# Performance work log

Measured on AMD Instinct MI355X. Metric: run time of the kernel, lower is better.

The kernel has to match this reference:

```python
import jax, jax.numpy as jnp
import numpy as np

T_STEPS = 100
T_EMB = 16
EPS = 1e-8


def sin_emb(t, dim):
    # sinusoidal_time_embedding: [cos(t*f), sin(t*f)] with f = exp(-log(1e4)*i/half)
    half = dim // 2
    freqs = jnp.exp(-jnp.log(jnp.float32(10000.0)) * jnp.arange(half, dtype=jnp.float32) / half)
    a = t.astype(jnp.float32)[:, None] * freqs[None, :]
    return jnp.concatenate([jnp.cos(a), jnp.sin(a)], axis=-1)


def lstm_layer(x_tbf, W_ih, W_hh, b):
    # x_tbf: [T, B, F]; torch gate order i, f, g, o
    B = x_tbf.shape[1]
    H = W_hh.shape[1]

    def step(carry, x_t):
        h, c = carry
        g = x_t @ W_ih.T + h @ W_hh.T + b
        i, f, gg, o = jnp.split(g, 4, axis=-1)
        c = jax.nn.sigmoid(f) * c + jax.nn.sigmoid(i) * jnp.tanh(gg)
        h = jax.nn.sigmoid(o) * jnp.tanh(c)
        return (h, c), h

    z = jnp.zeros((B, H), x_tbf.dtype)
    (h, c), ys = jax.lax.scan(step, (z, z), x_tbf)
    return ys, h


def _forward(x_hist, x_future, y0, turb_idx, pred_steps, init_noise, turb_emb,
             W_ih0, W_hh0, b_ih0, b_hh0, W_ih1, W_hh1, b_ih1, b_hh1,
             W1, b1, W2, b2, W3, b3):
    betas = jnp.linspace(1e-4, 0.02, T_STEPS).astype(jnp.float32)
    alphas = 1.0 - betas
    alpha_bars = jnp.cumprod(alphas)

    B = x_hist.shape[0]
    emb = turb_emb[turb_idx]  # [B, E]
    eh = jnp.broadcast_to(emb[:, None, :], (B, x_hist.shape[1], emb.shape[1]))
    ef = jnp.broadcast_to(emb[:, None, :], (B, x_future.shape[1], emb.shape[1]))
    xh = jnp.concatenate([x_hist, eh], axis=-1).transpose(1, 0, 2)    # [T_in, B, F+E]
    xf = jnp.concatenate([x_future, ef], axis=-1).transpose(1, 0, 2)  # [P, B, exo+E]

    ys0, _ = lstm_layer(xh, W_ih0, W_hh0, b_ih0 + b_hh0)
    _, enc_out = lstm_layer(ys0, W_ih1, W_hh1, b_ih1 + b_hh1)         # [B, H] = h[-1]

    def mlp(x):
        h = jax.nn.relu(x @ W1.T + b1)
        h = jax.nn.relu(h @ W2.T + b2)
        return h @ W3.T + b3

    def ar_step(prev_y, xs):
        exo_t, step, y_init = xs
        cond = jnp.concatenate([enc_out, exo_t, prev_y], axis=1)  # [B, cond_dim]
        h_e = sin_emb(jnp.full((B,), step), T_EMB)

        def dstep(y, t):
            t_e = sin_emb(jnp.full((B,), t), T_EMB)
            eps_hat = mlp(jnp.concatenate([cond, y, t_e, h_e], axis=1))  # [B,1]
            b_t, a_t, ab_t = betas[t], alphas[t], alpha_bars[t]
            pred_x0 = (y - jnp.sqrt(1.0 - ab_t) * eps_hat) / (jnp.sqrt(ab_t) + EPS)
            mean = (y - b_t / (jnp.sqrt(1.0 - ab_t) + EPS) * eps_hat) / (jnp.sqrt(a_t) + EPS)
            # eval mode -> deterministic sampling: posterior noise term is zero
            return jnp.where(t == 0, pred_x0, mean), None

        y, _ = jax.lax.scan(dstep, y_init, jnp.arange(T_STEPS - 1, -1, -1))
        return y, y[:, 0]

    _, seq = jax.lax.scan(ar_step, y0, (xf, jnp.arange(pred_steps), init_noise))
    return seq.T[:, :, None]  # [B, pred_steps, 1]


def setup_inputs() -> dict:
    key = jax.random.key(0)
    ks = list(jax.random.split(key, 24))
    kit = iter(ks)
    B, T_IN, F_IN, EXO, EMB, PRED, HID, NTURB = 1024, 96, 8, 6, 16, 8, 128, 100
    in0 = F_IN + EMB                 # 24
    cond_dim = HID + EXO + EMB + 1   # 151
    in_mlp = cond_dim + 1 + T_EMB + T_EMB  # 184

    def nrm(shape, s=0.05):
        return jax.random.normal(next(kit), shape, jnp.float32) * s

    return {
        'x_hist': jax.random.normal(next(kit), (B, T_IN, F_IN), jnp.float32),
        'x_future': jax.random.normal(next(kit), (B, PRED, EXO), jnp.float32),
        'y0': jnp.zeros((B, 1), jnp.float32),
        'turb_idx': jax.random.randint(next(kit), (B,), 0, NTURB),
        'pred_steps': PRED,
        'init_noise': jax.random.normal(next(kit), (PRED, B, 1), jnp.float32),
        'turb_emb': nrm((NTURB, EMB), 0.1),
        'W_ih0': nrm((4 * HID, in0)), 'W_hh0': nrm((4 * HID, HID)),
        'b_ih0': jnp.zeros((4 * HID,), jnp.float32), 'b_hh0': jnp.zeros((4 * HID,), jnp.float32),
        'W_ih1': nrm((4 * HID, HID)), 'W_hh1': nrm((4 * HID, HID)),
        'b_ih1': jnp.zeros((4 * HID,), jnp.float32), 'b_hh1': jnp.zeros((4 * HID,), jnp.float32),
        'W1': nrm((HID, in_mlp)), 'b1': jnp.zeros((HID,), jnp.float32),
        'W2': nrm((HID, HID)), 'b2': jnp.zeros((HID,), jnp.float32),
        'W3': nrm((1, HID)), 'b3': jnp.zeros((1,), jnp.float32),
    }


def reference(x_hist, x_future, y0, turb_idx, pred_steps, init_noise, turb_emb,
              W_ih0, W_hh0, b_ih0, b_hh0, W_ih1, W_hh1, b_ih1, b_hh1,
              W1, b1, W2, b2, W3, b3):
    return _forward(x_hist, x_future, y0, turb_idx, pred_steps, init_noise, turb_emb,
                    W_ih0, W_hh0, b_ih0, b_hh0, W_ih1, W_hh1, b_ih1, b_hh1,
                    W1, b1, W2, b2, W3, b3)
```

## Files before the change

kernel.cpp:

```cpp
#include <hip/hip_runtime.h>
#include <hip/hip_fp16.h>
#include <stdint.h>


typedef __attribute__((ext_vector_type(2))) _Float16 half2_t;
typedef __attribute__((ext_vector_type(8))) _Float16 v8h;
typedef __attribute__((ext_vector_type(4))) float v4f;

#define DEV __device__ __forceinline__

DEV uint32_t pack2f(float a, float b) {
  __half ha = __float2half_rn(a), hb = __float2half_rn(b);
  return (uint32_t)__half_as_ushort(ha) | ((uint32_t)__half_as_ushort(hb) << 16);
}

DEV float2 up2(uint32_t u) {
  half2_t h = __builtin_bit_cast(half2_t, u);
  return make_float2((float)h.x, (float)h.y);
}

DEV float fast_ex2(float x) {
#if __has_builtin(__builtin_amdgcn_exp2f)
  return __builtin_amdgcn_exp2f(x);
#else
  return exp2f(x);
#endif
}
DEV float fast_rcp(float x) {
#if __has_builtin(__builtin_amdgcn_rcpf)
  return __builtin_amdgcn_rcpf(x);
#else
  return 1.f / x;
#endif
}
DEV float sigm(float x) { return fast_rcp(1.f + fast_ex2(-1.4426950408889634f * x)); }
DEV float tanh_f(float x) {
  return 2.f * fast_rcp(1.f + fast_ex2(-2.8853900817779268f * x)) - 1.f;
}

DEV uint32_t pk_add(uint32_t a, uint32_t b) {
  return __builtin_bit_cast(uint32_t,
      __builtin_bit_cast(half2_t, a) + __builtin_bit_cast(half2_t, b));
}

DEV uint32_t pk_relufma(uint32_t w, uint32_t y, uint32_t b) {
  half2_t r = __builtin_bit_cast(half2_t, w) * __builtin_bit_cast(half2_t, y) +
              __builtin_bit_cast(half2_t, b);
  half2_t z = {(_Float16)0.f, (_Float16)0.f};
#if __has_builtin(__builtin_elementwise_max)
  r = __builtin_elementwise_max(r, z);
#else
  uint32_t u = __builtin_bit_cast(uint32_t, r);
  uint32_t mask = ((u >> 15) & 1u) * 0xFFFFu | ((u >> 31) & 1u) * 0xFFFF0000u;
  r = __builtin_bit_cast(half2_t, u & ~mask);
#endif
  return __builtin_bit_cast(uint32_t, r);
}

DEV uint32_t pk_max0(uint32_t a) {
  half2_t z = {(_Float16)0.f, (_Float16)0.f};
#if __has_builtin(__builtin_elementwise_max)
  return __builtin_bit_cast(uint32_t,
      __builtin_elementwise_max(__builtin_bit_cast(half2_t, a), z));
#else
  uint32_t mask = ((a >> 15) & 1u) * 0xFFFFu | ((a >> 31) & 1u) * 0xFFFF0000u;
  return a & ~mask;
#endif
}

DEV uint32_t cvtpk(float y) {
#if __has_builtin(__builtin_amdgcn_cvt_pkrtz)
  return __builtin_bit_cast(uint32_t, __builtin_amdgcn_cvt_pkrtz(y, y));
#else
  return pack2f(y, y);
#endif
}

DEV uint32_t cvtpk2(float a, float b) {
#if __has_builtin(__builtin_amdgcn_cvt_pkrtz)
  return __builtin_bit_cast(uint32_t, __builtin_amdgcn_cvt_pkrtz(a, b));
#else
  return pack2f(a, b);
#endif
}

DEV half2_t pk_fma2(uint32_t a, uint32_t b, half2_t c) {
  return __builtin_bit_cast(half2_t, a) * __builtin_bit_cast(half2_t, b) + c;
}

static constexpr size_t OFF_XH  = 0;
static constexpr size_t OFF_W0  = 4718592;
static constexpr size_t OFF_BS0 = 4882432;
static constexpr size_t OFF_W1L = 4884480;
static constexpr size_t OFF_BS1 = 5146624;
static constexpr size_t OFF_W2P = 5148672;
static constexpr size_t OFF_ENC = 5181440;
static constexpr size_t OFF_YS0 = 5705728;

__global__ void k_prep_xh(const float* __restrict__ xh, const int* __restrict__ tix,
                          const float* __restrict__ temb, uint32_t* __restrict__ out) {
  int idx = blockIdx.x * 256 + threadIdx.x;
  if (idx >= 96 * 1024 * 12) return;
  int m = idx % 12;
  int tb = idx / 12;
  int b = tb & 1023, t = tb >> 10;
  int k0 = 2 * m, k1 = k0 + 1;
  float v0 = (k0 < 8) ? xh[(b * 96 + t) * 8 + k0] : temb[tix[b] * 16 + (k0 - 8)];
  float v1 = (k1 < 8) ? xh[(b * 96 + t) * 8 + k1] : temb[tix[b] * 16 + (k1 - 8)];
  out[idx] = pack2f(v0, v1);
}

__global__ void k_prep_w(const float* __restrict__ Wih0, const float* __restrict__ Whh0,
                         const float* __restrict__ bih0, const float* __restrict__ bhh0,
                         const float* __restrict__ Wih1, const float* __restrict__ Whh1,
                         const float* __restrict__ bih1, const float* __restrict__ bhh1,
                         const float* __restrict__ W2,
                         uint32_t* __restrict__ w0p, uint32_t* __restrict__ w1p,
                         uint32_t* __restrict__ w2p, float* __restrict__ bs0,
                         float* __restrict__ bs1) {
  int idx = blockIdx.x * 256 + threadIdx.x;
  if (idx < 40960) {
    int w = idx / 5120;
    int r = idx % 5120;
    int T = r / 1280; r %= 1280;
    int f = r / 256;  r %= 256;
    int l = r >> 2, c = r & 3;
    int m = l & 15, qf = l >> 4;
    int g = (m & 3) * 128 + w * 16 + (m >> 2) * 4 + T;
    int k0 = f * 32 + qf * 8 + 2 * c, k1 = k0 + 1;
    float a = (k0 < 24) ? Wih0[g * 24 + k0] : ((k0 < 152) ? Whh0[g * 128 + k0 - 24] : 0.f);
    float b = (k1 < 24) ? Wih0[g * 24 + k1] : ((k1 < 152) ? Whh0[g * 128 + k1 - 24] : 0.f);
    w0p[idx] = pack2f(a, b);
  } else if (idx < 106496) {
    int i = idx - 40960;
    int w = i / 8192;
    int r = i % 8192;
    int T = r / 2048; r %= 2048;
    int f = r / 256;  r %= 256;
    int l = r >> 2, c = r & 3;
    int m = l & 15, qf = l >> 4;
    int g = (m & 3) * 128 + w * 16 + (m >> 2) * 4 + T;
    int k0 = f * 32 + qf * 8 + 2 * c, k1 = k0 + 1;
    float a = (k0 < 128) ? Wih1[g * 128 + k0] : Whh1[g * 128 + k0 - 128];
    float b = (k1 < 128) ? Wih1[g * 128 + k1] : Whh1[g * 128 + k1 - 128];
    w1p[i] = pack2f(a, b);
  } else if (idx < 114688) {
    int i = idx - 106496;
    w2p[i] = pack2f(W2[2 * i], W2[2 * i + 1]);
  } else if (idx < 115200) {
    int i = idx - 114688;
    bs0[i] = bih0[i] + bhh0[i];
  } else if (idx < 115712) {
    int i = idx - 115200;
    bs1[i] = bih1[i] + bhh1[i];
  }
}

__global__ __launch_bounds__(512, 2) void k_lstm0(const uint32_t* __restrict__ xh16,
                                                  const uint32_t* __restrict__ w0A,
                                                  const float* __restrict__ bs0,
                                                  __half* __restrict__ ys0) {
  __shared__ __align__(16) __half inb[2][16][160];
  const int tid = threadIdx.x;
  const int w = tid >> 6, l = tid & 63;
  const int n = l & 15, ql = l >> 4;
  const int ju = w * 16 + ql * 4;
  const int bbase = blockIdx.x * 16;

  uint4 Af[4][5];
#pragma unroll
  for (int T = 0; T < 4; T++)
#pragma unroll
    for (int f = 0; f < 5; f++)
      Af[T][f] = ((const uint4*)w0A)[((w * 4 + T) * 5 + f) * 64 + l];
  float bias[4][4];
#pragma unroll
  for (int T = 0; T < 4; T++)
#pragma unroll
    for (int r = 0; r < 4; r++) bias[T][r] = bs0[r * 128 + ju + T];

  for (int i = tid; i < 2560; i += 512) ((uint32_t*)inb)[i] = 0u;
  __syncthreads();
  if (tid < 192) {
    int b = tid / 12, m = tid % 12;
    ((uint32_t*)&inb[0][b][0])[m] = xh16[(0 * 1024 + bbase + b) * 12 + m];
  }
  float cst[4] = {0.f, 0.f, 0.f, 0.f};
  __syncthreads();

  for (int t = 0; t < 96; t++) {
    const int cur = t & 1, nxt = cur ^ 1;
    uint32_t sx = 0;
    int sb = 0, sm = 0;
    if (t < 95 && tid < 192) {
      sb = tid / 12; sm = tid % 12;
      sx = xh16[((t + 1) * 1024 + bbase + sb) * 12 + sm];
    }
    v4f acc[4];
#pragma unroll
    for (int T = 0; T < 4; T++) acc[T] = (v4f){0.f, 0.f, 0.f, 0.f};
#pragma unroll
    for (int f = 0; f < 5; f++) {
      uint4 bu = *(const uint4*)&inb[cur][n][f * 32 + ql * 8];
      v8h Bv = __builtin_bit_cast(v8h, bu);
#pragma unroll
      for (int T = 0; T < 4; T++)
        acc[T] = __builtin_amdgcn_mfma_f32_16x16x32_f16(
            __builtin_bit_cast(v8h, Af[T][f]), Bv, acc[T], 0, 0, 0);
    }
    float hv[4];
#pragma unroll
    for (int T = 0; T < 4; T++) {
      float gi = acc[T][0] + bias[T][0];
      float gf = acc[T][1] + bias[T][1];
      float gg = acc[T][2] + bias[T][2];
      float go = acc[T][3] + bias[T][3];
      float c = sigm(gf) * cst[T] + sigm(gi) * tanh_f(gg);
      cst[T] = c;
      hv[T] = sigm(go) * tanh_f(c);
    }
    uint32_t h01 = pack2f(hv[0], hv[1]), h23 = pack2f(hv[2], hv[3]);
    *(uint2*)&inb[nxt][n][24 + ju] = make_uint2(h01, h23);
    *(uint2*)((__half*)ys0 + (size_t)(t * 1024 + bbase + n) * 128 + ju) = make_uint2(h01, h23);
    if (t < 95 && tid < 192) ((uint32_t*)&inb[nxt][sb][0])[sm] = sx;
    __syncthreads();
  }
}

__global__ __launch_bounds__(512, 2) void k_lstm1(const uint32_t* __restrict__ ys0u,
                                                  const uint32_t* __restrict__ w1A,
                                                  const float* __restrict__ bs1,
                                                  float* __restrict__ enc) {
  __shared__ __align__(16) __half inb[2][16][264];
  const int tid = threadIdx.x;
  const int w = tid >> 6, l = tid & 63;
  const int n = l & 15, ql = l >> 4;
  const int ju = w * 16 + ql * 4;
  const int bbase = blockIdx.x * 16;
  const int sb = tid >> 5, sc = tid & 31;

  uint4 Af[4][8];
#pragma unroll
  for (int T = 0; T < 4; T++)
#pragma unroll
    for (int f = 0; f < 8; f++)
      Af[T][f] = ((const uint4*)w1A)[((w * 4 + T) * 8 + f) * 64 + l];
  float bias[4][4];
#pragma unroll
  for (int T = 0; T < 4; T++)
#pragma unroll
    for (int r = 0; r < 4; r++) bias[T][r] = bs1[r * 128 + ju + T];

  for (int i = tid; i < 4224; i += 512) ((uint32_t*)inb)[i] = 0u;
  __syncthreads();
  {
    uint2 v = ((const uint2*)ys0u)[(size_t)(0 * 1024 + bbase + sb) * 32 + sc];
    *(uint2*)&inb[0][sb][sc * 4] = v;
  }
  float cst[4] = {0.f, 0.f, 0.f, 0.f};
  __syncthreads();

  for (int t = 0; t < 96; t++) {
    const int cur = t & 1, nxt = cur ^ 1;
    uint2 sv = make_uint2(0u, 0u);
    if (t < 95)
      sv = ((const uint2*)ys0u)[(size_t)((t + 1) * 1024 + bbase + sb) * 32 + sc];
    v4f acc[4];
#pragma unroll
    for (int T = 0; T < 4; T++) acc[T] = (v4f){0.f, 0.f, 0.f, 0.f};
#pragma unroll
    for (int f = 0; f < 8; f++) {
      uint4 bu = *(const uint4*)&inb[cur][n][f * 32 + ql * 8];
      v8h Bv = __builtin_bit_cast(v8h, bu);
#pragma unroll
      for (int T = 0; T < 4; T++)
        acc[T] = __builtin_amdgcn_mfma_f32_16x16x32_f16(
            __builtin_bit_cast(v8h, Af[T][f]), Bv, acc[T], 0, 0, 0);
    }
    float hv[4];
#pragma unroll
    for (int T = 0; T < 4; T++) {
      float gi = acc[T][0] + bias[T][0];
      float gf = acc[T][1] + bias[T][1];
      float gg = acc[T][2] + bias[T][2];
      float go = acc[T][3] + bias[T][3];
      float c = sigm(gf) * cst[T] + sigm(gi) * tanh_f(gg);
      cst[T] = c;
      hv[T] = sigm(go) * tanh_f(c);
    }
    *(uint2*)&inb[nxt][n][128 + ju] = make_uint2(pack2f(hv[0], hv[1]), pack2f(hv[2], hv[3]));
    if (t < 95) *(uint2*)&inb[nxt][sb][sc * 4] = sv;
    if (t == 95)
      *(float4*)&enc[(size_t)(bbase + n) * 128 + ju] = make_float4(hv[0], hv[1], hv[2], hv[3]);
    __syncthreads();
  }
}

__global__ __launch_bounds__(64, 1) void k_diff(
    const float* __restrict__ xfut, const float* __restrict__ y0,
    const int* __restrict__ tix, const float* __restrict__ noise,
    const float* __restrict__ temb, const float* __restrict__ W1,
    const float* __restrict__ b1, const float* __restrict__ b2,
    const float* __restrict__ W3, const float* __restrict__ b3,
    const uint32_t* __restrict__ w2p, const float* __restrict__ enc,
    float* __restrict__ out) {
  __shared__ uint32_t W1sL[128 * 65];
  __shared__ uint32_t W1xL[128 * 29];
  __shared__ uint32_t encPL[16 * 65];
  __shared__ uint32_t embPL[16 * 9];
  __shared__ float teL[100][16];
  __shared__ float2 ccL[100];
  __shared__ __align__(16) __half tprojL[100 * 128];
  __shared__ __half hprojL[8 * 128];
  __shared__ uint32_t encdL[64 * 17];
  __shared__ __align__(16) uint4 w2Lv[16 * 64];

  const int tid = threadIdx.x;
  const int l = tid;
  const int m = l & 15, q = l >> 4;
  const int gbase = blockIdx.x * 16;

  for (int i = tid; i < 128 * 64; i += 64) {
    int r = i >> 6, c = i & 63;
    W1sL[r * 65 + c] = pack2f(W1[r * 184 + 2 * c], W1[r * 184 + 2 * c + 1]);
  }
  for (int i = tid; i < 128 * 28; i += 64) {
    int r = i / 28, c = i % 28;
    W1xL[r * 29 + c] = pack2f(W1[r * 184 + 128 + 2 * c], W1[r * 184 + 129 + 2 * c]);
  }
  for (int i = tid; i < 16 * 64; i += 64) {
    int bq = i >> 6, c = i & 63;
    encPL[bq * 65 + c] = pack2f(enc[(gbase + bq) * 128 + 2 * c],
                                enc[(gbase + bq) * 128 + 2 * c + 1]);
  }
  for (int i = tid; i < 16 * 8; i += 64) {
    int bq = i >> 3, c = i & 7;
    const float* er = temb + tix[gbase + bq] * 16;
    embPL[bq * 9 + c] = pack2f(er[2 * c], er[2 * c + 1]);
  }
  for (int p = tid; p < 1600; p += 64) {
    int tt = p >> 4, i = p & 15;
    float f = expf(-logf(10000.f) * (float)(i & 7) / 8.f);
    float a = (float)tt * f;
    teL[tt][i] = (i < 8) ? cosf(a) : sinf(a);
  }
  for (int qq = tid; qq < 100; qq += 64) {
    float ab = 1.f, beta = 0.f;
    for (int i = 0; i <= qq; i++) {
      beta = 1e-4f + (0.02f - 1e-4f) * (float)i / 99.f;
      ab *= (1.f - beta);
    }
    float cs, cd;
    if (qq == 0) { cs = sqrtf(1.f - ab); cd = 1.f / (sqrtf(ab) + 1e-8f); }
    else { cs = beta / (sqrtf(1.f - ab) + 1e-8f); cd = 1.f / (sqrtf(1.f - beta) + 1e-8f); }
    ccL[qq] = make_float2(cs, cd);
  }
  {
    const uint4* w2u4 = (const uint4*)w2p;
#pragma unroll
    for (int tt = 0; tt < 4; tt++)
#pragma unroll
      for (int f = 0; f < 4; f++)
        w2Lv[(tt * 4 + f) * 64 + l] = w2u4[((tt + 4) * 16 + m) * 16 + f * 4 + q];
  }
  __syncthreads();

#pragma unroll
  for (int kk = 0; kk < 2; kk++) {
    int k = tid + kk * 64;
    float wte[16], whe[16];
#pragma unroll
    for (int i = 0; i < 8; i++) {
      float2 a = up2(W1xL[k * 29 + 12 + i]);
      wte[2 * i] = a.x; wte[2 * i + 1] = a.y;
      float2 bqq = up2(W1xL[k * 29 + 20 + i]);
      whe[2 * i] = bqq.x; whe[2 * i + 1] = bqq.y;
    }
    for (int tt = 0; tt < 100; tt++) {
      float s = 0.f;
#pragma unroll
      for (int i = 0; i < 16; i++) s += wte[i] * teL[tt][i];
      tprojL[tt * 128 + k] = __float2half_rn(s);
    }
    for (int ss = 0; ss < 8; ss++) {
      float s = 0.f;
#pragma unroll
      for (int i = 0; i < 16; i++) s += whe[i] * teL[ss][i];
      hprojL[ss * 128 + k] = __float2half_rn(s);
    }
  }

  for (int pi = 0; pi < 16; pi++) {
    int k0 = (pi >> 2) * 32 + q * 8 + (pi & 3) * 2;
    half2_t a0 = {(_Float16)0.f, (_Float16)0.f};
    half2_t a1 = a0;
    const uint32_t* wr0 = &W1sL[k0 * 65];
    const uint32_t* wr1 = &W1sL[(k0 + 1) * 65];
    const uint32_t* ep = &encPL[m * 65];
#pragma unroll 8
    for (int c = 0; c < 64; c++) {
      half2_t e = __builtin_bit_cast(half2_t, ep[c]);
      a0 += __builtin_bit_cast(half2_t, wr0[c]) * e;
      a1 += __builtin_bit_cast(half2_t, wr1[c]) * e;
    }
#pragma unroll
    for (int c = 0; c < 8; c++) {
      half2_t e = __builtin_bit_cast(half2_t, embPL[m * 9 + c]);
      a0 += __builtin_bit_cast(half2_t, W1xL[k0 * 29 + 3 + c]) * e;
      a1 += __builtin_bit_cast(half2_t, W1xL[(k0 + 1) * 29 + 3 + c]) * e;
    }
    float e0 = b1[k0] + (float)a0.x + (float)a0.y;
    float e1 = b1[k0 + 1] + (float)a1.x + (float)a1.y;
    encdL[tid * 17 + pi] = pack2f(e0, e1);
  }

  uint4 Bf[4][4];
  {
    const uint4* w2u4 = (const uint4*)w2p;
#pragma unroll
    for (int tt = 0; tt < 4; tt++)
#pragma unroll
      for (int f = 0; f < 4; f++) Bf[tt][f] = w2u4[(tt * 16 + m) * 16 + f * 4 + q];
  }
  uint32_t b2P[16], w3P[16];
#pragma unroll
  for (int tt = 0; tt < 8; tt++) {
    b2P[2 * tt]     = pack2f(b2[tt * 16 + q * 4 + 0], b2[tt * 16 + q * 4 + 1]);
    b2P[2 * tt + 1] = pack2f(b2[tt * 16 + q * 4 + 2], b2[tt * 16 + q * 4 + 3]);
    w3P[2 * tt]     = pack2f(W3[tt * 16 + q * 4 + 0], W3[tt * 16 + q * 4 + 1]);
    w3P[2 * tt + 1] = pack2f(W3[tt * 16 + q * 4 + 2], W3[tt * 16 + q * 4 + 3]);
  }
  const float b3v = b3[0];
  const int bpaddr = (l ^ 32) << 2;

  uint32_t w1yP[16];
#pragma unroll
  for (int pi = 0; pi < 16; pi++) {
    int k0 = (pi >> 2) * 32 + q * 8 + (pi & 3) * 2;
    uint32_t ua = W1xL[k0 * 29 + 11];
    uint32_t ub = W1xL[(k0 + 1) * 29 + 11];
    w1yP[pi] = (ua >> 16) | (ub & 0xFFFF0000u);
  }

  float prev_y = y0[gbase + m];
  __syncthreads();

  float y = 0.f;
  float2 ccv = make_float2(0.f, 0.f);
  uint32_t bph[16], bt[16];
  const v4f zf = (v4f){0.f, 0.f, 0.f, 0.f};

#define DSTEP(t_)                                                              \
  do {                                                                         \
                           \
    uint4 L45[2][4];                                                           \
    _Pragma("unroll")                                                          \
    for (int tt = 0; tt < 2; tt++)                                             \
      _Pragma("unroll")                                                        \
      for (int f = 0; f < 4; f++) L45[tt][f] = w2Lv[(tt * 4 + f) * 64 + l];    \
    const uint32_t yP = cvtpk(y);                                              \
    uint4 au[4];                                                               \
    _Pragma("unroll")                                                          \
    for (int f = 0; f < 4; f++) {                                              \
      au[f].x = pk_relufma(w1yP[4 * f + 0], yP, bt[4 * f + 0]);                \
      au[f].y = pk_relufma(w1yP[4 * f + 1], yP, bt[4 * f + 1]);                \
      au[f].z = pk_relufma(w1yP[4 * f + 2], yP, bt[4 * f + 2]);                \
      au[f].w = pk_relufma(w1yP[4 * f + 3], yP, bt[4 * f + 3]);                \
    }                                                                          \
    v4f acc[8];                                                                \
    _Pragma("unroll")                                                          \
    for (int tt = 0; tt < 4; tt++)                                             \
      acc[tt] = __builtin_amdgcn_mfma_f32_16x16x32_f16(                        \
          __builtin_bit_cast(v8h, Bf[tt][0]), __builtin_bit_cast(v8h, au[0]),  \
          zf, 0, 0, 0);                                                        \
    _Pragma("unroll")                                                          \
    for (int f = 1; f < 4; f++)                                                \
      _Pragma("unroll")                                                        \
      for (int tt = 0; tt < 4; tt++)                                           \
        acc[tt] = __builtin_amdgcn_mfma_f32_16x16x32_f16(                      \
            __builtin_bit_cast(v8h, Bf[tt][f]), __builtin_bit_cast(v8h, au[f]),\
            acc[tt], 0, 0, 0);                                                 \
    uint4 L67[2][4];                                                           \
    _Pragma("unroll")                                                          \
    for (int tt = 0; tt < 2; tt++)                                             \
      _Pragma("unroll")                                                        \
      for (int f = 0; f < 4; f++) L67[tt][f] = w2Lv[((tt + 2) * 4 + f) * 64 + l]; \
    _Pragma("unroll")                                                          \
    for (int tt = 0; tt < 2; tt++)                                             \
      acc[4 + tt] = __builtin_amdgcn_mfma_f32_16x16x32_f16(                    \
          __builtin_bit_cast(v8h, L45[tt][0]), __builtin_bit_cast(v8h, au[0]), \
          zf, 0, 0, 0);                                                        \
    _Pragma("unroll")                                                          \
    for (int f = 1; f < 4; f++)                                                \
      _Pragma("unroll")                                                        \
      for (int tt = 0; tt < 2; tt++)                                           \
        acc[4 + tt] = __builtin_amdgcn_mfma_f32_16x16x32_f16(                  \
            __builtin_bit_cast(v8h, L45[tt][f]), __builtin_bit_cast(v8h, au[f]),\
            acc[4 + tt], 0, 0, 0);                                             \
    _Pragma("unroll")                                                          \
    for (int tt = 0; tt < 2; tt++)                                             \
      acc[6 + tt] = __builtin_amdgcn_mfma_f32_16x16x32_f16(                    \
          __builtin_bit_cast(v8h, L67[tt][0]), __builtin_bit_cast(v8h, au[0]), \
          zf, 0, 0, 0);                                                        \
    _Pragma("unroll")                                                          \
    for (int f = 1; f < 4; f++)                                                \
      _Pragma("unroll")                                                        \
      for (int tt = 0; tt < 2; tt++)                                           \
        acc[6 + tt] = __builtin_amdgcn_mfma_f32_16x16x32_f16(                  \
            __builtin_bit_cast(v8h, L67[tt][f]), __builtin_bit_cast(v8h, au[f]),\
            acc[6 + tt], 0, 0, 0);                                             \
    const int tn_ = ((t_) > 0) ? (t_) - 1 : 0;                                 \
    const uint4* tb_ = (const uint4*)(tprojL + tn_ * 128 + q * 8);             \
    uint4 t0 = tb_[0], t1 = tb_[4], t2 = tb_[8], t3 = tb_[12];                 \
    float2 ccn_ = ccL[tn_];                                                    \
    half2_t run01 = {(_Float16)0.f, (_Float16)0.f};                            \
    half2_t run23 = run01;                                                     \
    _Pragma("unroll")                                                          \
    for (int tt = 0; tt < 8; tt++) {                                           \
      uint32_t h01 = pk_max0(pk_add(cvtpk2(acc[tt][0], acc[tt][1]), b2P[2 * tt]));     \
      uint32_t h23 = pk_max0(pk_add(cvtpk2(acc[tt][2], acc[tt][3]), b2P[2 * tt + 1])); \
      run01 = pk_fma2(h01, w3P[2 * tt], run01);                                \
      run23 = pk_fma2(h23, w3P[2 * tt + 1], run23);                            \
    }                                                                          \
    float sv = ((float)run01.x + (float)run01.y) +                             \
               ((float)run23.x + (float)run23.y);                              \
    sv += __builtin_bit_cast(float, __builtin_amdgcn_ds_swizzle(               \
              __builtin_bit_cast(int, sv), 0x401F));                           \
    sv += __builtin_bit_cast(float, __builtin_amdgcn_ds_bpermute(              \
              bpaddr, __builtin_bit_cast(int, sv)));                           \
    y = (y - ccv.x * (b3v + sv)) * ccv.y;                                      \
    ccv = ccn_;                                                                \
    bt[0] = pk_add(bph[0], t0.x);   bt[1] = pk_add(bph[1], t0.y);              \
    bt[2] = pk_add(bph[2], t0.z);   bt[3] = pk_add(bph[3], t0.w);              \
    bt[4] = pk_add(bph[4], t1.x);   bt[5] = pk_add(bph[5], t1.y);              \
    bt[6] = pk_add(bph[6], t1.z);   bt[7] = pk_add(bph[7], t1.w);              \
    bt[8] = pk_add(bph[8], t2.x);   bt[9] = pk_add(bph[9], t2.y);              \
    bt[10] = pk_add(bph[10], t2.z); bt[11] = pk_add(bph[11], t2.w);            \
    bt[12] = pk_add(bph[12], t3.x); bt[13] = pk_add(bph[13], t3.y);            \
    bt[14] = pk_add(bph[14], t3.z); bt[15] = pk_add(bph[15], t3.w);            \
  } while (0)

  for (int s = 0; s < 8; s++) {
    float yn = noise[s * 1024 + gbase + m];
    float xf[6];
#pragma unroll
    for (int i = 0; i < 6; i++) xf[i] = xfut[((gbase + m) * 8 + s) * 6 + i];
#pragma unroll
    for (int pi = 0; pi < 16; pi++) {
      int k0 = (pi >> 2) * 32 + q * 8 + (pi & 3) * 2;
      float2 ed = up2(encdL[tid * 17 + pi]);
      float e0 = ed.x, e1 = ed.y;
#pragma unroll
      for (int c = 0; c < 3; c++) {
        float2 w0v = up2(W1xL[k0 * 29 + c]);
        float2 w1v = up2(W1xL[(k0 + 1) * 29 + c]);
        e0 += w0v.x * xf[2 * c] + w0v.y * xf[2 * c + 1];
        e1 += w1v.x * xf[2 * c] + w1v.y * xf[2 * c + 1];
      }
      e0 += up2(W1xL[k0 * 29 + 11]).x * prev_y;
      e1 += up2(W1xL[(k0 + 1) * 29 + 11]).x * prev_y;
      e0 += (float)hprojL[s * 128 + k0];
      e1 += (float)hprojL[s * 128 + k0 + 1];
      bph[pi] = pack2f(e0, e1);
    }

    y = yn;
    {
      const uint4* tb = (const uint4*)(tprojL + 99 * 128 + q * 8);
      uint4 t0 = tb[0], t1 = tb[4], t2 = tb[8], t3 = tb[12];
      bt[0] = pk_add(bph[0], t0.x);   bt[1] = pk_add(bph[1], t0.y);
      bt[2] = pk_add(bph[2], t0.z);   bt[3] = pk_add(bph[3], t0.w);
      bt[4] = pk_add(bph[4], t1.x);   bt[5] = pk_add(bph[5], t1.y);
      bt[6] = pk_add(bph[6], t1.z);   bt[7] = pk_add(bph[7], t1.w);
      bt[8] = pk_add(bph[8], t2.x);   bt[9] = pk_add(bph[9], t2.y);
      bt[10] = pk_add(bph[10], t2.z); bt[11] = pk_add(bph[11], t2.w);
      bt[12] = pk_add(bph[12], t3.x); bt[13] = pk_add(bph[13], t3.y);
      bt[14] = pk_add(bph[14], t3.z); bt[15] = pk_add(bph[15], t3.w);
    }
    ccv = ccL[99];

#pragma unroll 2
    for (int t = 99; t >= 0; --t) DSTEP(t);

    if (l < 16) out[(gbase + l) * 8 + s] = y;
    prev_y = y;
  }
#undef DSTEP
}

extern "C" void kernel_launch(void* const* d_in, const int* in_sizes, int n_in,
                              void* d_out, int out_size, void* d_ws, size_t ws_size,
                              hipStream_t stream) {
  const float* x_hist    = (const float*)d_in[0];
  const float* x_future  = (const float*)d_in[1];
  const float* y0        = (const float*)d_in[2];
  const int*   turb_idx  = (const int*)d_in[3];
  const float* init_noise = (const float*)d_in[5];
  const float* turb_emb  = (const float*)d_in[6];
  const float* W_ih0     = (const float*)d_in[7];
  const float* W_hh0     = (const float*)d_in[8];
  const float* b_ih0     = (const float*)d_in[9];
  const float* b_hh0     = (const float*)d_in[10];
  const float* W_ih1     = (const float*)d_in[11];
  const float* W_hh1     = (const float*)d_in[12];
  const float* b_ih1     = (const float*)d_in[13];
  const float* b_hh1     = (const float*)d_in[14];
  const float* W1        = (const float*)d_in[15];
  const float* b1        = (const float*)d_in[16];
  const float* W2        = (const float*)d_in[17];
  const float* b2        = (const float*)d_in[18];
  const float* W3        = (const float*)d_in[19];
  const float* b3        = (const float*)d_in[20];

  char* ws = (char*)d_ws;
  uint32_t* xh16 = (uint32_t*)(ws + OFF_XH);
  uint32_t* w0p  = (uint32_t*)(ws + OFF_W0);
  float*    bs0  = (float*)(ws + OFF_BS0);
  uint32_t* w1p  = (uint32_t*)(ws + OFF_W1L);
  float*    bs1  = (float*)(ws + OFF_BS1);
  uint32_t* w2p  = (uint32_t*)(ws + OFF_W2P);
  float*    encf = (float*)(ws + OFF_ENC);
  __half*   ys0h = (__half*)(ws + OFF_YS0);

  k_prep_xh<<<4608, 256, 0, stream>>>(x_hist, turb_idx, turb_emb, xh16);
  k_prep_w<<<452, 256, 0, stream>>>(W_ih0, W_hh0, b_ih0, b_hh0,
                                    W_ih1, W_hh1, b_ih1, b_hh1,
                                    W2, w0p, w1p, w2p, bs0, bs1);
  k_lstm0<<<64, 512, 0, stream>>>(xh16, w0p, bs0, ys0h);
  k_lstm1<<<64, 512, 0, stream>>>((const uint32_t*)ys0h, w1p, bs1, encf);
  k_diff<<<64, 64, 0, stream>>>(x_future, y0, turb_idx, init_noise, turb_emb,
                                W1, b1, b2, W3, b3, w2p, encf, (float*)d_out);
}
```

Measured before the change: 776.0 us.

## Split diffusion MLP hidden layer across four waves with shared-memory reduction

The diffusion kernel goes from one wave to four waves per block. Each wave now computes a quarter of the second-layer MFMA output tiles, dropping from 32 MFMAs per step to 8, and holds only its own slice of W2 in registers instead of staging part of it in LDS. Per-wave partial outputs go to a double-buffered shared array. A __syncthreads and an LDS sum then rebuild eps each step. Every wave still repeats the first-layer and scalar update work, so the shorter per-step MFMA chain is paid for with a block barrier on each of the 800 sequential denoising steps.

```diff
diff --git a/kernel.cpp b/kernel.cpp
--- a/kernel.cpp
+++ b/kernel.cpp
@@ -296,7 +296,7 @@
   }
 }
 
-__global__ __launch_bounds__(64, 1) void k_diff(
+__global__ __launch_bounds__(256, 1) void k_diff(
     const float* __restrict__ xfut, const float* __restrict__ y0,
     const int* __restrict__ tix, const float* __restrict__ noise,
     const float* __restrict__ temb, const float* __restrict__ W1,
@@ -312,39 +312,39 @@
   __shared__ float2 ccL[100];
   __shared__ __align__(16) __half tprojL[100 * 128];
   __shared__ __half hprojL[8 * 128];
-  __shared__ uint32_t encdL[64 * 17];
-  __shared__ __align__(16) uint4 w2Lv[16 * 64];
+  __shared__ uint32_t encdL[256 * 17];
+  __shared__ __align__(16) float partL[2][16][20];
 
   const int tid = threadIdx.x;
-  const int l = tid;
+  const int w = tid >> 6, l = tid & 63;
   const int m = l & 15, q = l >> 4;
   const int gbase = blockIdx.x * 16;
 
-  for (int i = tid; i < 128 * 64; i += 64) {
+  for (int i = tid; i < 128 * 64; i += 256) {
     int r = i >> 6, c = i & 63;
     W1sL[r * 65 + c] = pack2f(W1[r * 184 + 2 * c], W1[r * 184 + 2 * c + 1]);
   }
-  for (int i = tid; i < 128 * 28; i += 64) {
+  for (int i = tid; i < 128 * 28; i += 256) {
     int r = i / 28, c = i % 28;
     W1xL[r * 29 + c] = pack2f(W1[r * 184 + 128 + 2 * c], W1[r * 184 + 129 + 2 * c]);
   }
-  for (int i = tid; i < 16 * 64; i += 64) {
+  for (int i = tid; i < 16 * 64; i += 256) {
     int bq = i >> 6, c = i & 63;
     encPL[bq * 65 + c] = pack2f(enc[(gbase + bq) * 128 + 2 * c],
                                 enc[(gbase + bq) * 128 + 2 * c + 1]);
   }
-  for (int i = tid; i < 16 * 8; i += 64) {
+  for (int i = tid; i < 16 * 8; i += 256) {
     int bq = i >> 3, c = i & 7;
     const float* er = temb + tix[gbase + bq] * 16;
     embPL[bq * 9 + c] = pack2f(er[2 * c], er[2 * c + 1]);
   }
-  for (int p = tid; p < 1600; p += 64) {
+  for (int p = tid; p < 1600; p += 256) {
     int tt = p >> 4, i = p & 15;
     float f = expf(-logf(10000.f) * (float)(i & 7) / 8.f);
     float a = (float)tt * f;
     teL[tt][i] = (i < 8) ? cosf(a) : sinf(a);
   }
-  for (int qq = tid; qq < 100; qq += 64) {
+  for (int qq = tid; qq < 100; qq += 256) {
     float ab = 1.f, beta = 0.f;
     for (int i = 0; i <= qq; i++) {
       beta = 1e-4f + (0.02f - 1e-4f) * (float)i / 99.f;
@@ -355,19 +355,10 @@
     else { cs = beta / (sqrtf(1.f - ab) + 1e-8f); cd = 1.f / (sqrtf(1.f - beta) + 1e-8f); }
     ccL[qq] = make_float2(cs, cd);
   }
+  __syncthreads();
+
   {
-    const uint4* w2u4 = (const uint4*)w2p;
-#pragma unroll
-    for (int tt = 0; tt < 4; tt++)
-#pragma unroll
-      for (int f = 0; f < 4; f++)
-        w2Lv[(tt * 4 + f) * 64 + l] = w2u4[((tt + 4) * 16 + m) * 16 + f * 4 + q];
-  }
-  __syncthreads();
-
-#pragma unroll
-  for (int kk = 0; kk < 2; kk++) {
-    int k = tid + kk * 64;
+    int k = tid & 127, hs = tid >> 7;
     float wte[16], whe[16];
 #pragma unroll
     for (int i = 0; i < 8; i++) {
@@ -376,17 +367,19 @@
       float2 bqq = up2(W1xL[k * 29 + 20 + i]);
       whe[2 * i] = bqq.x; whe[2 * i + 1] = bqq.y;
     }
-    for (int tt = 0; tt < 100; tt++) {
+    for (int tt = hs * 50; tt < hs * 50 + 50; tt++) {
       float s = 0.f;
 #pragma unroll
       for (int i = 0; i < 16; i++) s += wte[i] * teL[tt][i];
       tprojL[tt * 128 + k] = __float2half_rn(s);
     }
-    for (int ss = 0; ss < 8; ss++) {
-      float s = 0.f;
-#pragma unroll
-      for (int i = 0; i < 16; i++) s += whe[i] * teL[ss][i];
-      hprojL[ss * 128 + k] = __float2half_rn(s);
+    if (hs == 0) {
+      for (int ss = 0; ss < 8; ss++) {
+        float s = 0.f;
+#pragma unroll
+        for (int i = 0; i < 16; i++) s += whe[i] * teL[ss][i];
+        hprojL[ss * 128 + k] = __float2half_rn(s);
+      }
     }
   }
 
@@ -414,24 +407,26 @@
     encdL[tid * 17 + pi] = pack2f(e0, e1);
   }
 
-  uint4 Bf[4][4];
+  uint4 Bf[2][4];
   {
     const uint4* w2u4 = (const uint4*)w2p;
 #pragma unroll
-    for (int tt = 0; tt < 4; tt++)
-#pragma unroll
-      for (int f = 0; f < 4; f++) Bf[tt][f] = w2u4[(tt * 16 + m) * 16 + f * 4 + q];
-  }
-  uint32_t b2P[16], w3P[16];
-#pragma unroll
-  for (int tt = 0; tt < 8; tt++) {
-    b2P[2 * tt]     = pack2f(b2[tt * 16 + q * 4 + 0], b2[tt * 16 + q * 4 + 1]);
-    b2P[2 * tt + 1] = pack2f(b2[tt * 16 + q * 4 + 2], b2[tt * 16 + q * 4 + 3]);
-    w3P[2 * tt]     = pack2f(W3[tt * 16 + q * 4 + 0], W3[tt * 16 + q * 4 + 1]);
-    w3P[2 * tt + 1] = pack2f(W3[tt * 16 + q * 4 + 2], W3[tt * 16 + q * 4 + 3]);
+    for (int j = 0; j < 2; j++)
+#pragma unroll
+      for (int f = 0; f < 4; f++)
+        Bf[j][f] = w2u4[((2 * w + j) * 16 + m) * 16 + f * 4 + q];
+  }
+  uint32_t b2P[4], w3P[4];
+#pragma unroll
+  for (int j = 0; j < 2; j++) {
+    int tt = 2 * w + j;
+    b2P[2 * j]     = pack2f(b2[tt * 16 + q * 4 + 0], b2[tt * 16 + q * 4 + 1]);
+    b2P[2 * j + 1] = pack2f(b2[tt * 16 + q * 4 + 2], b2[tt * 16 + q * 4 + 3]);
+    w3P[2 * j]     = pack2f(W3[tt * 16 + q * 4 + 0], W3[tt * 16 + q * 4 + 1]);
+    w3P[2 * j + 1] = pack2f(W3[tt * 16 + q * 4 + 2], W3[tt * 16 + q * 4 + 3]);
   }
   const float b3v = b3[0];
-  const int bpaddr = (l ^ 32) << 2;
+  const int pslot = w * 4 + q;
 
   uint32_t w1yP[16];
 #pragma unroll
@@ -450,14 +445,12 @@
   uint32_t bph[16], bt[16];
   const v4f zf = (v4f){0.f, 0.f, 0.f, 0.f};
 
-#define DSTEP(t_)                                                              \
+#define DSTEP(t_, PB)                                                          \
   do {                                                                         \
-                           \
-    uint4 L45[2][4];                                                           \
-    _Pragma("unroll")                                                          \
-    for (int tt = 0; tt < 2; tt++)                                             \
-      _Pragma("unroll")                                                        \
-      for (int f = 0; f < 4; f++) L45[tt][f] = w2Lv[(tt * 4 + f) * 64 + l];    \
+    const int tn_ = ((t_) > 0) ? (t_) - 1 : 0;                                 \
+    const uint4* tb_ = (const uint4*)(tprojL + tn_ * 128 + q * 8);             \
+    uint4 t0 = tb_[0], t1 = tb_[4], t2 = tb_[8], t3 = tb_[12];                 \
+    float2 ccn_ = ccL[tn_];                                                    \
     const uint32_t yP = cvtpk(y);                                              \
     uint4 au[4];                                                               \
     _Pragma("unroll")                                                          \
@@ -467,69 +460,38 @@
       au[f].z = pk_relufma(w1yP[4 * f + 2], yP, bt[4 * f + 2]);                \
       au[f].w = pk_relufma(w1yP[4 * f + 3], yP, bt[4 * f + 3]);                \
     }                                                                          \
-    v4f acc[8];                                                                \
-    _Pragma("unroll")                                                          \
-    for (int tt = 0; tt < 4; tt++)                                             \
-      acc[tt] = __builtin_amdgcn_mfma_f32_16x16x32_f16(                        \
-          __builtin_bit_cast(v8h, Bf[tt][0]), __builtin_bit_cast(v8h, au[0]),  \
-          zf, 0, 0, 0);                                                        \
-    _Pragma("unroll")                                                          \
-    for (int f = 1; f < 4; f++)                                                \
-      _Pragma("unroll")                                                        \
-      for (int tt = 0; tt < 4; tt++)                                           \
-        acc[tt] = __builtin_amdgcn_mfma_f32_16x16x32_f16(                      \
-            __builtin_bit_cast(v8h, Bf[tt][f]), __builtin_bit_cast(v8h, au[f]),\
-            acc[tt], 0, 0, 0);                                                 \
-    uint4 L67[2][4];                                                           \
-    _Pragma("unroll")                                                          \
-    for (int tt = 0; tt < 2; tt++)                                             \
-      _Pragma("unroll")                                                        \
-      for (int f = 0; f < 4; f++) L67[tt][f] = w2Lv[((tt + 2) * 4 + f) * 64 + l]; \
-    _Pragma("unroll")                                                          \
-    for (int tt = 0; tt < 2; tt++)                                             \
-      acc[4 + tt] = __builtin_amdgcn_mfma_f32_16x16x32_f16(                    \
-          __builtin_bit_cast(v8h, L45[tt][0]), __builtin_bit_cast(v8h, au[0]), \
-          zf, 0, 0, 0);                                                        \
-    _Pragma("unroll")                                                          \
-    for (int f = 1; f < 4; f++)                                                \
-      _Pragma("unroll")                                                        \
-      for (int tt = 0; tt < 2; tt++)                                           \
-        acc[4 + tt] = __builtin_amdgcn_mfma_f32_16x16x32_f16(                  \
-            __builtin_bit_cast(v8h, L45[tt][f]), __builtin_bit_cast(v8h, au[f]),\
-            acc[4 + tt], 0, 0, 0);                                             \
-    _Pragma("unroll")                                                          \
-    for (int tt = 0; tt < 2; tt++)                                             \
-      acc[6 + tt] = __builtin_amdgcn_mfma_f32_16x16x32_f16(                    \
-          __builtin_bit_cast(v8h, L67[tt][0]), __builtin_bit_cast(v8h, au[0]), \
-          zf, 0, 0, 0);                                                        \
-    _Pragma("unroll")                                                          \
-    for (int f = 1; f < 4; f++)                                                \
-      _Pragma("unroll")                                                        \
-      for (int tt = 0; tt < 2; tt++)                                           \
-        acc[6 + tt] = __builtin_amdgcn_mfma_f32_16x16x32_f16(                  \
-            __builtin_bit_cast(v8h, L67[tt][f]), __builtin_bit_cast(v8h, au[f]),\
-            acc[6 + tt], 0, 0, 0);                                             \
-    const int tn_ = ((t_) > 0) ? (t_) - 1 : 0;                                 \
-    const uint4* tb_ = (const uint4*)(tprojL + tn_ * 128 + q * 8);             \
-    uint4 t0 = tb_[0], t1 = tb_[4], t2 = tb_[8], t3 = tb_[12];                 \
-    float2 ccn_ = ccL[tn_];                                                    \
-    half2_t run01 = {(_Float16)0.f, (_Float16)0.f};                            \
-    half2_t run23 = run01;                                                     \
-    _Pragma("unroll")                                                          \
-    for (int tt = 0; tt < 8; tt++) {                                           \
-      uint32_t h01 = pk_max0(pk_add(cvtpk2(acc[tt][0], acc[tt][1]), b2P[2 * tt]));     \
-      uint32_t h23 = pk_max0(pk_add(cvtpk2(acc[tt][2], acc[tt][3]), b2P[2 * tt + 1])); \
-      run01 = pk_fma2(h01, w3P[2 * tt], run01);                                \
-      run23 = pk_fma2(h23, w3P[2 * tt + 1], run23);                            \
+                             \
+    v4f a0 = __builtin_amdgcn_mfma_f32_16x16x32_f16(                           \
+        __builtin_bit_cast(v8h, Bf[0][0]), __builtin_bit_cast(v8h, au[0]), zf, 0, 0, 0); \
+    v4f b0 = __builtin_amdgcn_mfma_f32_16x16x32_f16(                           \
+        __builtin_bit_cast(v8h, Bf[0][1]), __builtin_bit_cast(v8h, au[1]), zf, 0, 0, 0); \
+    v4f a1 = __builtin_amdgcn_mfma_f32_16x16x32_f16(                           \
+        __builtin_bit_cast(v8h, Bf[1][0]), __builtin_bit_cast(v8h, au[0]), zf, 0, 0, 0); \
+    v4f b1x = __builtin_amdgcn_mfma_f32_16x16x32_f16(                          \
+        __builtin_bit_cast(v8h, Bf[1][1]), __builtin_bit_cast(v8h, au[1]), zf, 0, 0, 0); \
+    a0 = __builtin_amdgcn_mfma_f32_16x16x32_f16(                               \
+        __builtin_bit_cast(v8h, Bf[0][2]), __builtin_bit_cast(v8h, au[2]), a0, 0, 0, 0); \
+    b0 = __builtin_amdgcn_mfma_f32_16x16x32_f16(                               \
+        __builtin_bit_cast(v8h, Bf[0][3]), __builtin_bit_cast(v8h, au[3]), b0, 0, 0, 0); \
+    a1 = __builtin_amdgcn_mfma_f32_16x16x32_f16(                               \
+        __builtin_bit_cast(v8h, Bf[1][2]), __builtin_bit_cast(v8h, au[2]), a1, 0, 0, 0); \
+    b1x = __builtin_amdgcn_mfma_f32_16x16x32_f16(                              \
+        __builtin_bit_cast(v8h, Bf[1][3]), __builtin_bit_cast(v8h, au[3]), b1x, 0, 0, 0); \
+    v4f c0 = a0 + b0, c1 = a1 + b1x;                                           \
+              \
+    half2_t run = {(_Float16)0.f, (_Float16)0.f};                              \
+    {                                                                          \
+      uint32_t h01 = pk_max0(pk_add(cvtpk2(c0[0], c0[1]), b2P[0]));            \
+      uint32_t h23 = pk_max0(pk_add(cvtpk2(c0[2], c0[3]), b2P[1]));            \
+      run = pk_fma2(h01, w3P[0], run);                                         \
+      run = pk_fma2(h23, w3P[1], run);                                         \
+      uint32_t g01 = pk_max0(pk_add(cvtpk2(c1[0], c1[1]), b2P[2]));            \
+      uint32_t g23 = pk_max0(pk_add(cvtpk2(c1[2], c1[3]), b2P[3]));            \
+      run = pk_fma2(g01, w3P[2], run);                                         \
+      run = pk_fma2(g23, w3P[3], run);                                         \
     }                                                                          \
-    float sv = ((float)run01.x + (float)run01.y) +                             \
-               ((float)run23.x + (float)run23.y);                              \
-    sv += __builtin_bit_cast(float, __builtin_amdgcn_ds_swizzle(               \
-              __builtin_bit_cast(int, sv), 0x401F));                           \
-    sv += __builtin_bit_cast(float, __builtin_amdgcn_ds_bpermute(              \
-              bpaddr, __builtin_bit_cast(int, sv)));                           \
-    y = (y - ccv.x * (b3v + sv)) * ccv.y;                                      \
-    ccv = ccn_;                                                                \
+    partL[PB][m][pslot] = (float)run.x + (float)run.y;                         \
+                                         \
     bt[0] = pk_add(bph[0], t0.x);   bt[1] = pk_add(bph[1], t0.y);              \
     bt[2] = pk_add(bph[2], t0.z);   bt[3] = pk_add(bph[3], t0.w);              \
     bt[4] = pk_add(bph[4], t1.x);   bt[5] = pk_add(bph[5], t1.y);              \
@@ -538,6 +500,13 @@
     bt[10] = pk_add(bph[10], t2.z); bt[11] = pk_add(bph[11], t2.w);            \
     bt[12] = pk_add(bph[12], t3.x); bt[13] = pk_add(bph[13], t3.y);            \
     bt[14] = pk_add(bph[14], t3.z); bt[15] = pk_add(bph[15], t3.w);            \
+    __syncthreads();                                                           \
+    const v4f* pl_ = (const v4f*)&partL[PB][m][0];                             \
+    v4f p0_ = pl_[0], p1_ = pl_[1], p2_ = pl_[2], p3_ = pl_[3];                \
+    v4f ps_ = (p0_ + p1_) + (p2_ + p3_);                                       \
+    float eps_ = b3v + ((ps_[0] + ps_[1]) + (ps_[2] + ps_[3]));                \
+    y = (y - ccv.x * eps_) * ccv.y;                                            \
+    ccv = ccn_;                                                                \
   } while (0)
 
   for (int s = 0; s < 8; s++) {
@@ -579,10 +548,12 @@
     }
     ccv = ccL[99];
 
-#pragma unroll 2
-    for (int t = 99; t >= 0; --t) DSTEP(t);
-
-    if (l < 16) out[(gbase + l) * 8 + s] = y;
+    for (int it = 0; it < 50; it++) {
+      DSTEP(99 - 2 * it, 0);
+      DSTEP(98 - 2 * it, 1);
+    }
+
+    if (w == 0 && l < 16) out[(gbase + l) * 8 + s] = y;
     prev_y = y;
   }
 #undef DSTEP
@@ -628,6 +599,6 @@
                                     W2, w0p, w1p, w2p, bs0, bs1);
   k_lstm0<<<64, 512, 0, stream>>>(xh16, w0p, bs0, ys0h);
   k_lstm1<<<64, 512, 0, stream>>>((const uint32_t*)ys0h, w1p, bs1, encf);
-  k_diff<<<64, 64, 0, stream>>>(x_future, y0, turb_idx, init_noise, turb_emb,
-                                W1, b1, b2, W3, b3, w2p, encf, (float*)d_out);
-}
+  k_diff<<<64, 256, 0, stream>>>(x_future, y0, turb_idx, init_noise, turb_emb,
+                                 W1, b1, b2, W3, b3, w2p, encf, (float*)d_out);
+}
```

After: 638.5 us. 1.22x faster.
